# Optimization experiments

Hardware: AMD Instinct MI355X
Metric: run time of the kernel (lower is better)

## Reference

```python
import jax, jax.numpy as jnp
import numpy as np

B, S_BERT, L_WORD, D = 64, 512, 256, 768
REDUC, HID, TAGS, POL = 400, 100, 5, 4


def _make_positions():
    # Each word spans 1-2 consecutive subwords; 256 words * max 2 <= 512 subwords.
    rng = np.random.default_rng(0)
    lens = rng.integers(1, 3, size=(B, L_WORD))          # [B, L] in {1,2}
    starts = np.cumsum(lens, axis=1) - lens              # exclusive prefix sum
    ends = starts + lens - 1                             # inclusive end, <= 511
    return jnp.asarray(np.stack([starts, ends], axis=-1), dtype=jnp.int32)


def setup_inputs() -> dict:
    key = jax.random.key(0)
    ks = jax.random.split(key, 8)
    s = 0.02
    return {
        "bert_vectors": jax.random.normal(ks[0], (B, S_BERT, D), jnp.float32),
        "positions": _make_positions(),
        "W_reduc": jax.random.normal(ks[1], (D, REDUC), jnp.float32) * s,
        "b_reduc": jnp.zeros((REDUC,), jnp.float32),
        "W_ap": jax.random.normal(ks[2], (REDUC, HID), jnp.float32) * s,
        "b_ap": jnp.zeros((HID,), jnp.float32),
        "W_op": jax.random.normal(ks[3], (REDUC, HID), jnp.float32) * s,
        "b_op": jnp.zeros((HID,), jnp.float32),
        "W_ap_tag": jax.random.normal(ks[4], (HID, TAGS), jnp.float32) * s,
        "b_ap_tag": jnp.zeros((TAGS,), jnp.float32),
        "W_op_tag": jax.random.normal(ks[5], (HID, TAGS), jnp.float32) * s,
        "b_op_tag": jnp.zeros((TAGS,), jnp.float32),
        # Biaffine: bias=(True, False) -> in1 gets a ones column: [HID+1, POL*HID]
        "W_bi": jax.random.normal(ks[6], (HID + 1, POL * HID), jnp.float32) * s,
    }


def _segment_mean(vectors, positions):
    # vectors: [B, S, D]; positions: [B, L, 2] inclusive (start, end) spans.
    cs = jnp.cumsum(vectors, axis=1)
    cs = jnp.concatenate([jnp.zeros_like(cs[:, :1]), cs], axis=1)   # [B, S+1, D]
    starts = positions[..., 0]
    ends = positions[..., 1]
    hi = jnp.take_along_axis(cs, (ends + 1)[..., None], axis=1)     # [B, L, D]
    lo = jnp.take_along_axis(cs, starts[..., None], axis=1)
    lens = (ends - starts + 1).astype(vectors.dtype)[..., None]
    return (hi - lo) / lens                                          # [B, L, D]


def reference(bert_vectors, positions, W_reduc, b_reduc, W_ap, b_ap, W_op, b_op,
              W_ap_tag, b_ap_tag, W_op_tag, b_op_tag, W_bi):
    pooled = _segment_mean(bert_vectors, positions)                  # [B, L, D]
    h = jax.nn.relu(pooled @ W_reduc + b_reduc)                      # [B, L, 400]
    ap = jax.nn.relu(h @ W_ap + b_ap)                                # [B, L, 100]
    op = jax.nn.relu(h @ W_op + b_op)                                # [B, L, 100]
    ap_out = ap @ W_ap_tag + b_ap_tag                                # [B, L, T]
    op_out = op @ W_op_tag + b_op_tag                                # [B, L, T]
    # Biaffine with bias=(True, False)
    ones = jnp.ones_like(ap[..., :1])
    a1 = jnp.concatenate([ap, ones], axis=-1)                        # [B, L, 101]
    affine = (a1 @ W_bi).reshape(ap.shape[0], ap.shape[1], POL, HID) # [B, L1, P, H]
    triplet = jnp.einsum('biph,bjh->bjip', affine, op)               # [B, L2, L1, P]
    return ap_out, op_out, triplet
```

## Files before the change

kernel.cpp:

```cpp
#include <hip/hip_runtime.h>
#include <hip/hip_bf16.h>

#define B_    64
#define S_    512
#define L_    256
#define D_    768
#define RED_  400
#define REDP_ 512
#define HID_  100
#define HIDP_ 128
#define TAGS_ 5
#define POL_  4
#define NBI_  512
#define NAO_  256
#define BL_   (B_ * L_)

typedef __attribute__((ext_vector_type(8))) short short8;
typedef __attribute__((ext_vector_type(4))) float f32x4;
typedef __attribute__((ext_vector_type(4))) unsigned short u16x4;

#define GLOAD_LDS16(gp, lp) __builtin_amdgcn_global_load_lds( \
    (const __attribute__((address_space(1))) void*)(gp),      \
    (__attribute__((address_space(3))) void*)(lp), 16, 0, 0)

__device__ inline float bf2f(unsigned short u) {
    union { unsigned int i; float f; } c; c.i = ((unsigned)u) << 16; return c.f;
}
__device__ inline unsigned short f2bf(float f) {
    __hip_bfloat16 h = __float2bfloat16(f);
    unsigned short u;
    __builtin_memcpy(&u, &h, 2);
    return u;
}

#define SZ0 393216
#define SZ1 131072
#define SZ2 65536
#define SZ3 512
#define SZ4 256
#define PREP_TOT (SZ0 + SZ1 + SZ2 + SZ3 + SZ4)
#define SEG_BLOCKS (BL_ / 4)
#define PREP_BLOCKS ((PREP_TOT + 255) / 256)

__global__ __launch_bounds__(256) void front_kernel(
    const float* __restrict__ bert, const int* __restrict__ pos,
    unsigned short* __restrict__ pooled,
    const float* __restrict__ W_reduc, const float* __restrict__ b_reduc,
    const float* __restrict__ W_ap, const float* __restrict__ b_ap,
    const float* __restrict__ W_op, const float* __restrict__ b_op,
    const float* __restrict__ W_bi,
    unsigned short* __restrict__ WtR, unsigned short* __restrict__ WtAO,
    unsigned short* __restrict__ WtBi,
    float* __restrict__ bR, float* __restrict__ bAO, float* __restrict__ bBi)
{
    if (blockIdx.x < SEG_BLOCKS) {
        int r  = threadIdx.x >> 6;
        int l  = threadIdx.x & 63;
        int bl = blockIdx.x * 4 + r;
        int b  = bl >> 8;
        int s  = pos[bl * 2 + 0];
        int e  = pos[bl * 2 + 1];
        int len = e - s + 1;
        const float* v0 = bert + ((size_t)b * S_ + s) * D_;
        float inv = (len == 2) ? 0.5f : 1.0f;
        unsigned short* outp = pooled + (size_t)bl * D_;
        #pragma unroll
        for (int c = 0; c < 3; ++c) {
            int d = l * 4 + c * 256;
            f32x4 x = *(const f32x4*)(v0 + d);
            if (len == 2) {
                f32x4 y = *(const f32x4*)(v0 + D_ + d);
                x += y;
            }
            u16x4 o;
            #pragma unroll
            for (int j = 0; j < 4; ++j) o[j] = f2bf(x[j] * inv);
            *(u16x4*)(outp + d) = o;
        }
        return;
    }

    int idx = (blockIdx.x - SEG_BLOCKS) * 256 + threadIdx.x;
    if (idx < SZ0) {
        int n = idx / D_, k = idx - n * D_;
        float v = (n < RED_) ? W_reduc[(size_t)k * RED_ + n] : 0.f;
        WtR[idx] = f2bf(v);
    } else if (idx < SZ0 + SZ1) {
        int i = idx - SZ0;
        int n = i >> 9, k = i & 511;
        float v = 0.f;
        if (k < RED_) {
            if (n < HID_)                      v = W_ap[(size_t)k * HID_ + n];
            else if (n >= 128 && n < 128+HID_) v = W_op[(size_t)k * HID_ + (n-128)];
        }
        WtAO[i] = f2bf(v);
    } else if (idx < SZ0 + SZ1 + SZ2) {
        int i = idx - SZ0 - SZ1;
        int n = i >> 7, k = i & 127;
        int p = n >> 7, h = n & 127;
        float v = (h < HID_ && k < HID_) ? W_bi[(size_t)k * RED_ + p * HID_ + h] : 0.f;
        WtBi[i] = f2bf(v);
        if (k == 0) bBi[n] = (h < HID_) ? W_bi[(size_t)HID_ * RED_ + p * HID_ + h] : 0.f;
    } else if (idx < SZ0 + SZ1 + SZ2 + SZ3) {
        int n = idx - SZ0 - SZ1 - SZ2;
        bR[n] = (n < RED_) ? b_reduc[n] : 0.f;
    } else if (idx < PREP_TOT) {
        int n = idx - SZ0 - SZ1 - SZ2 - SZ3;
        bAO[n] = (n < 128) ? ((n < HID_) ? b_ap[n] : 0.f)
                           : (((n-128) < HID_) ? b_op[n-128] : 0.f);
    }
}

__global__ __launch_bounds__(256) void gemm1_kernel(
    const short* __restrict__ A, const short* __restrict__ Bt,
    const float* __restrict__ bias, unsigned short* __restrict__ Co,
    int M, int N, int K)
{
    __shared__ __align__(16) short lds[2][8192];

    const int t  = threadIdx.x;
    const int wv = t >> 6;
    const int ln = t & 63;
    const int wm = wv >> 1;
    const int wn = wv & 1;
    const int bm = blockIdx.x * 128;
    const int bn = blockIdx.y * 128;

    const int srow = t >> 2;
    const int skc  = (t & 3) * 8;

    f32x4 acc[4][4] = {};
    const int NT = K >> 5;

    {
        #pragma unroll
        for (int q = 0; q < 2; ++q) {
            const short* g = A + (size_t)(bm + q * 64 + srow) * K + skc;
            GLOAD_LDS16(g, &lds[0][q * 2048 + wv * 512]);
        }
        #pragma unroll
        for (int q = 0; q < 2; ++q) {
            const short* g = Bt + (size_t)(bn + q * 64 + srow) * K + skc;
            GLOAD_LDS16(g, &lds[0][4096 + q * 2048 + wv * 512]);
        }
    }
    __syncthreads();

    int cur = 0;
    const int lr = ln & 15;
    const int lk = (ln >> 4) * 8;

    for (int kt = 0; kt < NT; ++kt) {
        if (kt + 1 < NT) {
            int k0 = (kt + 1) << 5;
            #pragma unroll
            for (int q = 0; q < 2; ++q) {
                const short* g = A + (size_t)(bm + q * 64 + srow) * K + k0 + skc;
                GLOAD_LDS16(g, &lds[cur ^ 1][q * 2048 + wv * 512]);
            }
            #pragma unroll
            for (int q = 0; q < 2; ++q) {
                const short* g = Bt + (size_t)(bn + q * 64 + srow) * K + k0 + skc;
                GLOAD_LDS16(g, &lds[cur ^ 1][4096 + q * 2048 + wv * 512]);
            }
        }

        const short* As = &lds[cur][0];
        const short* Bs = &lds[cur][4096];
        short8 a[4], b[4];
        #pragma unroll
        for (int fi = 0; fi < 4; ++fi)
            a[fi] = *(const short8*)(As + (wm * 64 + fi * 16 + lr) * 32 + lk);
        #pragma unroll
        for (int fj = 0; fj < 4; ++fj)
            b[fj] = *(const short8*)(Bs + (wn * 64 + fj * 16 + lr) * 32 + lk);
        #pragma unroll
        for (int fi = 0; fi < 4; ++fi)
            #pragma unroll
            for (int fj = 0; fj < 4; ++fj)
                acc[fi][fj] = __builtin_amdgcn_mfma_f32_16x16x32_bf16(
                    a[fi], b[fj], acc[fi][fj], 0, 0, 0);

        __syncthreads();
        cur ^= 1;
    }

    const int row0 = bm + wm * 64 + (ln >> 4) * 4;
    const int col0 = bn + wn * 64 + lr;
    #pragma unroll
    for (int fi = 0; fi < 4; ++fi)
        #pragma unroll
        for (int r = 0; r < 4; ++r) {
            int row = row0 + fi * 16 + r;
            #pragma unroll
            for (int fj = 0; fj < 4; ++fj) {
                int col = col0 + fj * 16;
                float v = fmaxf(acc[fi][fj][r] + bias[col], 0.f);
                Co[(size_t)row * N + col] = f2bf(v);
            }
        }
}

__global__ __launch_bounds__(256) void gemm23_tag_kernel(
    const short* __restrict__ A, const short* __restrict__ Bt,
    const float* __restrict__ bias,
    unsigned short* __restrict__ apOut, unsigned short* __restrict__ opOut,
    const float* __restrict__ Wap_tag, const float* __restrict__ bap_tag,
    const float* __restrict__ Wop_tag, const float* __restrict__ bop_tag,
    float* __restrict__ out_tag)
{
    __shared__ __align__(16) short lds[2][8192];
    __shared__ float tagf[128 * 101];
    __shared__ float Wtag[HID_ * TAGS_];
    __shared__ float Btag[TAGS_];

    const int t  = threadIdx.x;
    const int wv = t >> 6;
    const int ln = t & 63;
    const int wm = wv >> 1;
    const int wn = wv & 1;
    const int bm = blockIdx.x * 128;
    const int bn = blockIdx.y * 128;
    const int half = blockIdx.y;

    const float* Wt = half ? Wop_tag : Wap_tag;
    const float* bt = half ? bop_tag : bap_tag;
    for (int i = t; i < HID_ * TAGS_; i += 256) Wtag[i] = Wt[i];
    if (t < TAGS_) Btag[t] = bt[t];

    const int srow = t >> 2;
    const int skc  = (t & 3) * 8;
    const int K = REDP_;

    f32x4 acc[4][4] = {};

    {
        #pragma unroll
        for (int q = 0; q < 2; ++q) {
            const short* g = A + (size_t)(bm + q * 64 + srow) * K + skc;
            GLOAD_LDS16(g, &lds[0][q * 2048 + wv * 512]);
        }
        #pragma unroll
        for (int q = 0; q < 2; ++q) {
            const short* g = Bt + (size_t)(bn + q * 64 + srow) * K + skc;
            GLOAD_LDS16(g, &lds[0][4096 + q * 2048 + wv * 512]);
        }
    }
    __syncthreads();

    int cur = 0;
    const int lr = ln & 15;
    const int lk = (ln >> 4) * 8;

    for (int kt = 0; kt < 16; ++kt) {
        if (kt + 1 < 16) {
            int k0 = (kt + 1) << 5;
            #pragma unroll
            for (int q = 0; q < 2; ++q) {
                const short* g = A + (size_t)(bm + q * 64 + srow) * K + k0 + skc;
                GLOAD_LDS16(g, &lds[cur ^ 1][q * 2048 + wv * 512]);
            }
            #pragma unroll
            for (int q = 0; q < 2; ++q) {
                const short* g = Bt + (size_t)(bn + q * 64 + srow) * K + k0 + skc;
                GLOAD_LDS16(g, &lds[cur ^ 1][4096 + q * 2048 + wv * 512]);
            }
        }

        const short* As = &lds[cur][0];
        const short* Bs = &lds[cur][4096];
        short8 a[4], b[4];
        #pragma unroll
        for (int fi = 0; fi < 4; ++fi)
            a[fi] = *(const short8*)(As + (wm * 64 + fi * 16 + lr) * 32 + lk);
        #pragma unroll
        for (int fj = 0; fj < 4; ++fj)
            b[fj] = *(const short8*)(Bs + (wn * 64 + fj * 16 + lr) * 32 + lk);
        #pragma unroll
        for (int fi = 0; fi < 4; ++fi)
            #pragma unroll
            for (int fj = 0; fj < 4; ++fj)
                acc[fi][fj] = __builtin_amdgcn_mfma_f32_16x16x32_bf16(
                    a[fi], b[fj], acc[fi][fj], 0, 0, 0);

        __syncthreads();
        cur ^= 1;
    }

    unsigned short* Co = half ? opOut : apOut;
    const int rl0 = wm * 64 + (ln >> 4) * 4;
    const int cl0 = wn * 64 + lr;
    #pragma unroll
    for (int fi = 0; fi < 4; ++fi)
        #pragma unroll
        for (int r = 0; r < 4; ++r) {
            int rl = rl0 + fi * 16 + r;
            #pragma unroll
            for (int fj = 0; fj < 4; ++fj) {
                int cl = cl0 + fj * 16;
                float v = fmaxf(acc[fi][fj][r] + bias[bn + cl], 0.f);
                Co[(size_t)(bm + rl) * 128 + cl] = f2bf(v);
                if (cl < 101) tagf[rl * 101 + cl] = v;
            }
        }
    __syncthreads();

    if (t < 128) {
        float s[TAGS_];
        #pragma unroll
        for (int g = 0; g < TAGS_; ++g) s[g] = Btag[g];
        const float* rowp = &tagf[t * 101];
        for (int k = 0; k < HID_; ++k) {
            float x = rowp[k];
            #pragma unroll
            for (int g = 0; g < TAGS_; ++g) s[g] += x * Wtag[k * TAGS_ + g];
        }
        float* o = out_tag + (size_t)half * (BL_ * TAGS_) + (size_t)(bm + t) * TAGS_;
        #pragma unroll
        for (int g = 0; g < TAGS_; ++g) o[g] = s[g];
    }
}

__global__ __launch_bounds__(256) void affine_kernel(
    const short* __restrict__ ap, const short* __restrict__ WtBi,
    const float* __restrict__ bBi, unsigned short* __restrict__ affine)
{
    __shared__ __align__(16) short As[16384];
    __shared__ __align__(16) short Bs[16384];

    const int t  = threadIdx.x;
    const int wv = t >> 6;
    const int ln = t & 63;
    const int wm = wv >> 1;
    const int wn = wv & 1;
    const int bm = blockIdx.x * 128;
    const int bn = blockIdx.y * 128;

    const int rsub = ln >> 2;
    const int j8   = (ln & 3) * 8;

    #pragma unroll
    for (int i = 0; i < 8; ++i) {
        int ks = i >> 1, hf = i & 1;
        int rloc = wv * 32 + hf * 16;
        const short* gA = ap + (size_t)(bm + rloc + rsub) * HIDP_ + ks * 32 + j8;
        GLOAD_LDS16(gA, &As[ks * 4096 + rloc * 32]);
        const short* gB = WtBi + (size_t)(bn + rloc + rsub) * HIDP_ + ks * 32 + j8;
        GLOAD_LDS16(gB, &Bs[ks * 4096 + rloc * 32]);
    }
    __syncthreads();

    const int lr = ln & 15;
    const int lk = (ln >> 4) * 8;
    f32x4 acc[4][4] = {};

    #pragma unroll
    for (int ks = 0; ks < 4; ++ks) {
        short8 a[4], b[4];
        #pragma unroll
        for (int fi = 0; fi < 4; ++fi)
            a[fi] = *(const short8*)(As + ks * 4096 + (wm * 64 + fi * 16 + lr) * 32 + lk);
        #pragma unroll
        for (int fj = 0; fj < 4; ++fj)
            b[fj] = *(const short8*)(Bs + ks * 4096 + (wn * 64 + fj * 16 + lr) * 32 + lk);
        #pragma unroll
        for (int fi = 0; fi < 4; ++fi)
            #pragma unroll
            for (int fj = 0; fj < 4; ++fj)
                acc[fi][fj] = __builtin_amdgcn_mfma_f32_16x16x32_bf16(
                    a[fi], b[fj], acc[fi][fj], 0, 0, 0);
    }

    const int row0 = bm + wm * 64 + (ln >> 4) * 4;
    const int col0 = bn + wn * 64 + lr;
    #pragma unroll
    for (int fi = 0; fi < 4; ++fi)
        #pragma unroll
        for (int r = 0; r < 4; ++r) {
            int row = row0 + fi * 16 + r;
            #pragma unroll
            for (int fj = 0; fj < 4; ++fj) {
                int col = col0 + fj * 16;
                affine[(size_t)row * NBI_ + col] = f2bf(acc[fi][fj][r] + bBi[col]);
            }
        }
}

__global__ __launch_bounds__(256) void triplet_kernel(
    const short* __restrict__ op, const short* __restrict__ affine,
    float* __restrict__ out)
{
    __shared__ __align__(16) short As[16384];
    __shared__ __align__(16) short Bs[16384];

    const int t  = threadIdx.x;
    const int wv = t >> 6;
    const int ln = t & 63;
    const int wm = wv >> 1;
    const int wn = wv & 1;
    const int bm = blockIdx.x * 128;
    const int bn = blockIdx.y * 128;
    const int b  = blockIdx.z;

    const short* Ab = op     + (size_t)b * 256 * HIDP_;
    const short* Bb = affine + (size_t)b * 256 * NBI_;

    const int rsub = ln >> 2;
    const int j8   = (ln & 3) * 8;

    #pragma unroll
    for (int i = 0; i < 8; ++i) {
        int ks = i >> 1, hf = i & 1;
        int rloc = wv * 32 + hf * 16;
        const short* gA = Ab + (size_t)(bm + rloc + rsub) * HIDP_ + ks * 32 + j8;
        GLOAD_LDS16(gA, &As[ks * 4096 + rloc * 32]);
        int ip = bn + rloc + rsub;
        const short* gB = Bb + (size_t)(ip >> 2) * NBI_ + (ip & 3) * HIDP_ + ks * 32 + j8;
        GLOAD_LDS16(gB, &Bs[ks * 4096 + rloc * 32]);
    }
    __syncthreads();

    const int lr = ln & 15;
    const int lk = (ln >> 4) * 8;
    f32x4 acc[4][4] = {};

    #pragma unroll
    for (int ks = 0; ks < 4; ++ks) {
        short8 a[4], bf[4];
        #pragma unroll
        for (int fi = 0; fi < 4; ++fi)
            a[fi] = *(const short8*)(As + ks * 4096 + (wm * 64 + fi * 16 + lr) * 32 + lk);
        #pragma unroll
        for (int fj = 0; fj < 4; ++fj)
            bf[fj] = *(const short8*)(Bs + ks * 4096 + (wn * 64 + fj * 16 + lr) * 32 + lk);
        #pragma unroll
        for (int fi = 0; fi < 4; ++fi)
            #pragma unroll
            for (int fj = 0; fj < 4; ++fj)
                acc[fi][fj] = __builtin_amdgcn_mfma_f32_16x16x32_bf16(
                    a[fi], bf[fj], acc[fi][fj], 0, 0, 0);
    }

    float* O = out + (size_t)b * 256 * 1024;
    const int row0 = bm + wm * 64 + (ln >> 4) * 4;
    const int col0 = bn + wn * 64 + lr;
    #pragma unroll
    for (int fi = 0; fi < 4; ++fi)
        #pragma unroll
        for (int r = 0; r < 4; ++r) {
            int row = row0 + fi * 16 + r;
            #pragma unroll
            for (int fj = 0; fj < 4; ++fj)
                O[(size_t)row * 1024 + col0 + fj * 16] = acc[fi][fj][r];
        }
}

extern "C" void kernel_launch(void* const* d_in, const int* in_sizes, int n_in,
                              void* d_out, int out_size, void* d_ws, size_t ws_size,
                              hipStream_t stream)
{
    const float* bert     = (const float*)d_in[0];
    const int*   pos      = (const int*)  d_in[1];
    const float* W_reduc  = (const float*)d_in[2];
    const float* b_reduc  = (const float*)d_in[3];
    const float* W_ap     = (const float*)d_in[4];
    const float* b_ap     = (const float*)d_in[5];
    const float* W_op     = (const float*)d_in[6];
    const float* b_op     = (const float*)d_in[7];
    const float* W_ap_tag = (const float*)d_in[8];
    const float* b_ap_tag = (const float*)d_in[9];
    const float* W_op_tag = (const float*)d_in[10];
    const float* b_op_tag = (const float*)d_in[11];
    const float* W_bi     = (const float*)d_in[12];

    float* out = (float*)d_out;

    char* ws = (char*)d_ws;
    unsigned short* pooled = (unsigned short*)ws; ws += (size_t)BL_ * D_ * 2;
    unsigned short* h      = (unsigned short*)ws; ws += (size_t)BL_ * REDP_ * 2;
    unsigned short* ap     = (unsigned short*)ws; ws += (size_t)BL_ * HIDP_ * 2;
    unsigned short* opv    = (unsigned short*)ws; ws += (size_t)BL_ * HIDP_ * 2;
    unsigned short* affine = (unsigned short*)ws; ws += (size_t)BL_ * NBI_ * 2;
    unsigned short* WtR    = (unsigned short*)ws; ws += (size_t)REDP_ * D_ * 2;
    unsigned short* WtAO   = (unsigned short*)ws; ws += (size_t)NAO_ * REDP_ * 2;
    unsigned short* WtBi   = (unsigned short*)ws; ws += (size_t)NBI_ * HIDP_ * 2;
    float* bR  = (float*)ws;  ws += REDP_ * 4;
    float* bAO = (float*)ws;  ws += NAO_ * 4;
    float* bBi = (float*)ws;  ws += NBI_ * 4;

    front_kernel<<<SEG_BLOCKS + PREP_BLOCKS, 256, 0, stream>>>(
        bert, pos, pooled,
        W_reduc, b_reduc, W_ap, b_ap, W_op, b_op, W_bi,
        WtR, WtAO, WtBi, bR, bAO, bBi);

    gemm1_kernel<<<dim3(BL_ / 128, REDP_ / 128), 256, 0, stream>>>(
        (const short*)pooled, (const short*)WtR, bR, h, BL_, REDP_, D_);

    gemm23_tag_kernel<<<dim3(BL_ / 128, 2), 256, 0, stream>>>(
        (const short*)h, (const short*)WtAO, bAO, ap, opv,
        W_ap_tag, b_ap_tag, W_op_tag, b_op_tag, out);

    affine_kernel<<<dim3(BL_ / 128, NBI_ / 128), 256, 0, stream>>>(
        (const short*)ap, (const short*)WtBi, bBi, affine);

    triplet_kernel<<<dim3(2, 8, B_), 256, 0, stream>>>(
        (const short*)opv, (const short*)affine, out + 2 * BL_ * TAGS_);
}
```

Before: 84.50 us.

## Fuse biaffine projection into triplet kernel and skip padded GEMM columns

Removes the separate affine kernel and its large bf16 intermediate buffer. Each triplet block now computes its slice of the affine projection directly into LDS, from ap rows and WtBi, before running the op x affine MFMA. This saves a global write and read of the affine tensor plus one launch. The cost is that the two x-blocks sharing a slice both recompute it. Separately, gemm1 skips MFMAs and stores for output columns beyond 416, and gemm23 stops its K loop at 416 instead of 512, so less padded work is done.

```diff
diff --git a/kernel.cpp b/kernel.cpp
--- a/kernel.cpp
+++ b/kernel.cpp
@@ -7,6 +7,7 @@
 #define D_    768
 #define RED_  400
 #define REDP_ 512
+#define KEFF_ 416
 #define HID_  100
 #define HIDP_ 128
 #define TAGS_ 5
@@ -114,7 +115,7 @@
 __global__ __launch_bounds__(256) void gemm1_kernel(
     const short* __restrict__ A, const short* __restrict__ Bt,
     const float* __restrict__ bias, unsigned short* __restrict__ Co,
-    int M, int N, int K)
+    int M, int N, int K, int nlim)
 {
     __shared__ __align__(16) short lds[2][8192];
 
@@ -129,6 +130,9 @@
     const int srow = t >> 2;
     const int skc  = (t & 3) * 8;
 
+    int fjrem = (nlim - bn - wn * 64) >> 4;
+    const int fjcnt = fjrem < 0 ? 0 : (fjrem > 4 ? 4 : fjrem);
+
     f32x4 acc[4][4] = {};
     const int NT = K >> 5;
 
@@ -173,13 +177,15 @@
             a[fi] = *(const short8*)(As + (wm * 64 + fi * 16 + lr) * 32 + lk);
         #pragma unroll
         for (int fj = 0; fj < 4; ++fj)
-            b[fj] = *(const short8*)(Bs + (wn * 64 + fj * 16 + lr) * 32 + lk);
+            if (fj < fjcnt)
+                b[fj] = *(const short8*)(Bs + (wn * 64 + fj * 16 + lr) * 32 + lk);
         #pragma unroll
         for (int fi = 0; fi < 4; ++fi)
             #pragma unroll
             for (int fj = 0; fj < 4; ++fj)
-                acc[fi][fj] = __builtin_amdgcn_mfma_f32_16x16x32_bf16(
-                    a[fi], b[fj], acc[fi][fj], 0, 0, 0);
+                if (fj < fjcnt)
+                    acc[fi][fj] = __builtin_amdgcn_mfma_f32_16x16x32_bf16(
+                        a[fi], b[fj], acc[fi][fj], 0, 0, 0);
 
         __syncthreads();
         cur ^= 1;
@@ -193,11 +199,12 @@
         for (int r = 0; r < 4; ++r) {
             int row = row0 + fi * 16 + r;
             #pragma unroll
-            for (int fj = 0; fj < 4; ++fj) {
-                int col = col0 + fj * 16;
-                float v = fmaxf(acc[fi][fj][r] + bias[col], 0.f);
-                Co[(size_t)row * N + col] = f2bf(v);
-            }
+            for (int fj = 0; fj < 4; ++fj)
+                if (fj < fjcnt) {
+                    int col = col0 + fj * 16;
+                    float v = fmaxf(acc[fi][fj][r] + bias[col], 0.f);
+                    Co[(size_t)row * N + col] = f2bf(v);
+                }
         }
 }
 
@@ -230,19 +237,19 @@
 
     const int srow = t >> 2;
     const int skc  = (t & 3) * 8;
-    const int K = REDP_;
+    const int NT = KEFF_ >> 5;
 
     f32x4 acc[4][4] = {};
 
     {
         #pragma unroll
         for (int q = 0; q < 2; ++q) {
-            const short* g = A + (size_t)(bm + q * 64 + srow) * K + skc;
+            const short* g = A + (size_t)(bm + q * 64 + srow) * REDP_ + skc;
             GLOAD_LDS16(g, &lds[0][q * 2048 + wv * 512]);
         }
         #pragma unroll
         for (int q = 0; q < 2; ++q) {
-            const short* g = Bt + (size_t)(bn + q * 64 + srow) * K + skc;
+            const short* g = Bt + (size_t)(bn + q * 64 + srow) * REDP_ + skc;
             GLOAD_LDS16(g, &lds[0][4096 + q * 2048 + wv * 512]);
         }
     }
@@ -252,17 +259,17 @@
     const int lr = ln & 15;
     const int lk = (ln >> 4) * 8;
 
-    for (int kt = 0; kt < 16; ++kt) {
-        if (kt + 1 < 16) {
+    for (int kt = 0; kt < NT; ++kt) {
+        if (kt + 1 < NT) {
             int k0 = (kt + 1) << 5;
             #pragma unroll
             for (int q = 0; q < 2; ++q) {
-                const short* g = A + (size_t)(bm + q * 64 + srow) * K + k0 + skc;
+                const short* g = A + (size_t)(bm + q * 64 + srow) * REDP_ + k0 + skc;
                 GLOAD_LDS16(g, &lds[cur ^ 1][q * 2048 + wv * 512]);
             }
             #pragma unroll
             for (int q = 0; q < 2; ++q) {
-                const short* g = Bt + (size_t)(bn + q * 64 + srow) * K + k0 + skc;
+                const short* g = Bt + (size_t)(bn + q * 64 + srow) * REDP_ + k0 + skc;
                 GLOAD_LDS16(g, &lds[cur ^ 1][4096 + q * 2048 + wv * 512]);
             }
         }
@@ -321,77 +328,14 @@
     }
 }
 
-__global__ __launch_bounds__(256) void affine_kernel(
-    const short* __restrict__ ap, const short* __restrict__ WtBi,
-    const float* __restrict__ bBi, unsigned short* __restrict__ affine)
-{
-    __shared__ __align__(16) short As[16384];
-    __shared__ __align__(16) short Bs[16384];
-
-    const int t  = threadIdx.x;
-    const int wv = t >> 6;
-    const int ln = t & 63;
-    const int wm = wv >> 1;
-    const int wn = wv & 1;
-    const int bm = blockIdx.x * 128;
-    const int bn = blockIdx.y * 128;
-
-    const int rsub = ln >> 2;
-    const int j8   = (ln & 3) * 8;
-
-    #pragma unroll
-    for (int i = 0; i < 8; ++i) {
-        int ks = i >> 1, hf = i & 1;
-        int rloc = wv * 32 + hf * 16;
-        const short* gA = ap + (size_t)(bm + rloc + rsub) * HIDP_ + ks * 32 + j8;
-        GLOAD_LDS16(gA, &As[ks * 4096 + rloc * 32]);
-        const short* gB = WtBi + (size_t)(bn + rloc + rsub) * HIDP_ + ks * 32 + j8;
-        GLOAD_LDS16(gB, &Bs[ks * 4096 + rloc * 32]);
-    }
-    __syncthreads();
-
-    const int lr = ln & 15;
-    const int lk = (ln >> 4) * 8;
-    f32x4 acc[4][4] = {};
-
-    #pragma unroll
-    for (int ks = 0; ks < 4; ++ks) {
-        short8 a[4], b[4];
-        #pragma unroll
-        for (int fi = 0; fi < 4; ++fi)
-            a[fi] = *(const short8*)(As + ks * 4096 + (wm * 64 + fi * 16 + lr) * 32 + lk);
-        #pragma unroll
-        for (int fj = 0; fj < 4; ++fj)
-            b[fj] = *(const short8*)(Bs + ks * 4096 + (wn * 64 + fj * 16 + lr) * 32 + lk);
-        #pragma unroll
-        for (int fi = 0; fi < 4; ++fi)
-            #pragma unroll
-            for (int fj = 0; fj < 4; ++fj)
-                acc[fi][fj] = __builtin_amdgcn_mfma_f32_16x16x32_bf16(
-                    a[fi], b[fj], acc[fi][fj], 0, 0, 0);
-    }
-
-    const int row0 = bm + wm * 64 + (ln >> 4) * 4;
-    const int col0 = bn + wn * 64 + lr;
-    #pragma unroll
-    for (int fi = 0; fi < 4; ++fi)
-        #pragma unroll
-        for (int r = 0; r < 4; ++r) {
-            int row = row0 + fi * 16 + r;
-            #pragma unroll
-            for (int fj = 0; fj < 4; ++fj) {
-                int col = col0 + fj * 16;
-                affine[(size_t)row * NBI_ + col] = f2bf(acc[fi][fj][r] + bBi[col]);
-            }
-        }
-}
-
-__global__ __launch_bounds__(256) void triplet_kernel(
-    const short* __restrict__ op, const short* __restrict__ affine,
+__global__ __launch_bounds__(256) void bi_triplet_kernel(
+    const short* __restrict__ op, const short* __restrict__ ap,
+    const short* __restrict__ WtBi, const float* __restrict__ bBi,
     float* __restrict__ out)
 {
     __shared__ __align__(16) short As[16384];
     __shared__ __align__(16) short Bs[16384];
+    __shared__ __align__(16) short Aap[4096];
 
     const int t  = threadIdx.x;
     const int wv = t >> 6;
@@ -402,8 +346,8 @@
     const int bn = blockIdx.y * 128;
     const int b  = blockIdx.z;
 
-    const short* Ab = op     + (size_t)b * 256 * HIDP_;
-    const short* Bb = affine + (size_t)b * 256 * NBI_;
+    const short* opB = op + (size_t)b * 256 * HIDP_;
+    const short* apB = ap + ((size_t)b * 256 + blockIdx.y * 32) * HIDP_;
 
     const int rsub = ln >> 2;
     const int j8   = (ln & 3) * 8;
@@ -412,18 +356,59 @@
     for (int i = 0; i < 8; ++i) {
         int ks = i >> 1, hf = i & 1;
         int rloc = wv * 32 + hf * 16;
-        const short* gA = Ab + (size_t)(bm + rloc + rsub) * HIDP_ + ks * 32 + j8;
+        const short* gA = opB + (size_t)(bm + rloc + rsub) * HIDP_ + ks * 32 + j8;
         GLOAD_LDS16(gA, &As[ks * 4096 + rloc * 32]);
-        int ip = bn + rloc + rsub;
-        const short* gB = Bb + (size_t)(ip >> 2) * NBI_ + (ip & 3) * HIDP_ + ks * 32 + j8;
-        GLOAD_LDS16(gB, &Bs[ks * 4096 + rloc * 32]);
+    }
+    #pragma unroll
+    for (int q = 0; q < 2; ++q) {
+        int kf   = q * 2 + (wv >> 1);
+        int irow = (wv & 1) * 16 + (ln >> 2);
+        const short* gA = apB + (size_t)irow * HIDP_ + kf * 32 + (ln & 3) * 8;
+        GLOAD_LDS16(gA, &Aap[q * 2048 + wv * 512]);
     }
     __syncthreads();
 
     const int lr = ln & 15;
     const int lk = (ln >> 4) * 8;
+    const int hbase = wv * 32;
+
+    #pragma unroll
+    for (int p = 0; p < 4; ++p) {
+        f32x4 acc2[2][2] = {};
+        const short* Wp = WtBi + (size_t)(p * 128) * HIDP_;
+        #pragma unroll
+        for (int kf = 0; kf < 4; ++kf) {
+            short8 a2[2], b2[2];
+            #pragma unroll
+            for (int fm = 0; fm < 2; ++fm)
+                a2[fm] = *(const short8*)(Aap + kf * 1024 + (fm * 16 + lr) * 32 + lk);
+            #pragma unroll
+            for (int fn = 0; fn < 2; ++fn)
+                b2[fn] = *(const short8*)(Wp + (size_t)(hbase + fn * 16 + lr) * HIDP_ + kf * 32 + lk);
+            #pragma unroll
+            for (int fm = 0; fm < 2; ++fm)
+                #pragma unroll
+                for (int fn = 0; fn < 2; ++fn)
+                    acc2[fm][fn] = __builtin_amdgcn_mfma_f32_16x16x32_bf16(
+                        a2[fm], b2[fn], acc2[fm][fn], 0, 0, 0);
+        }
+        #pragma unroll
+        for (int fm = 0; fm < 2; ++fm)
+            #pragma unroll
+            for (int fn = 0; fn < 2; ++fn) {
+                int h = hbase + fn * 16 + lr;
+                float bias = bBi[p * 128 + h];
+                #pragma unroll
+                for (int r = 0; r < 4; ++r) {
+                    int i = fm * 16 + (ln >> 4) * 4 + r;
+                    float v = acc2[fm][fn][r] + bias;
+                    Bs[(h >> 5) * 4096 + (i * 4 + p) * 32 + (h & 31)] = (short)f2bf(v);
+                }
+            }
+    }
+    __syncthreads();
+
     f32x4 acc[4][4] = {};
-
     #pragma unroll
     for (int ks = 0; ks < 4; ++ks) {
         short8 a[4], bf[4];
@@ -480,7 +465,6 @@
     unsigned short* h      = (unsigned short*)ws; ws += (size_t)BL_ * REDP_ * 2;
     unsigned short* ap     = (unsigned short*)ws; ws += (size_t)BL_ * HIDP_ * 2;
     unsigned short* opv    = (unsigned short*)ws; ws += (size_t)BL_ * HIDP_ * 2;
-    unsigned short* affine = (unsigned short*)ws; ws += (size_t)BL_ * NBI_ * 2;
     unsigned short* WtR    = (unsigned short*)ws; ws += (size_t)REDP_ * D_ * 2;
     unsigned short* WtAO   = (unsigned short*)ws; ws += (size_t)NAO_ * REDP_ * 2;
     unsigned short* WtBi   = (unsigned short*)ws; ws += (size_t)NBI_ * HIDP_ * 2;
@@ -494,15 +478,13 @@
         WtR, WtAO, WtBi, bR, bAO, bBi);
 
     gemm1_kernel<<<dim3(BL_ / 128, REDP_ / 128), 256, 0, stream>>>(
-        (const short*)pooled, (const short*)WtR, bR, h, BL_, REDP_, D_);
+        (const short*)pooled, (const short*)WtR, bR, h, BL_, REDP_, D_, KEFF_);
 
     gemm23_tag_kernel<<<dim3(BL_ / 128, 2), 256, 0, stream>>>(
         (const short*)h, (const short*)WtAO, bAO, ap, opv,
         W_ap_tag, b_ap_tag, W_op_tag, b_op_tag, out);
 
-    affine_kernel<<<dim3(BL_ / 128, NBI_ / 128), 256, 0, stream>>>(
-        (const short*)ap, (const short*)WtBi, bBi, affine);
-
-    triplet_kernel<<<dim3(2, 8, B_), 256, 0, stream>>>(
-        (const short*)opv, (const short*)affine, out + 2 * BL_ * TAGS_);
-}
+    bi_triplet_kernel<<<dim3(2, 8, B_), 256, 0, stream>>>(
+        (const short*)opv, (const short*)ap, (const short*)WtBi, bBi,
+        out + 2 * BL_ * TAGS_);
+}
```

Result: slower. 96.48 us (+14.2%).

## Skip padded reduction columns in GEMMs and vectorize triplet output stores

Applied to the files above, without the earlier changes.

gemm1 now skips MFMAs, fragment loads and stores for output columns at or beyond 416, since the reduction width is 400 padded to 512. gemm23 iterates K only up to 416 instead of 512, saving 3 of 16 k-tiles. The triplet kernel swaps operand roles so each lane's accumulator holds four consecutive (i,p) outputs, allowing 16-byte vector stores instead of scalar strided stores. Columns 416-511 of h are left unwritten; this is safe only because gemm23 never reads past column 416, and it leaves uninitialized data in the workspace.

```diff
diff --git a/kernel.cpp b/kernel.cpp
--- a/kernel.cpp
+++ b/kernel.cpp
@@ -7,6 +7,7 @@
 #define D_    768
 #define RED_  400
 #define REDP_ 512
+#define KEFF_ 416
 #define HID_  100
 #define HIDP_ 128
 #define TAGS_ 5
@@ -114,7 +115,7 @@
 __global__ __launch_bounds__(256) void gemm1_kernel(
     const short* __restrict__ A, const short* __restrict__ Bt,
     const float* __restrict__ bias, unsigned short* __restrict__ Co,
-    int M, int N, int K)
+    int M, int N, int K, int nlim)
 {
     __shared__ __align__(16) short lds[2][8192];
 
@@ -129,6 +130,9 @@
     const int srow = t >> 2;
     const int skc  = (t & 3) * 8;
 
+    int fjrem = (nlim - bn - wn * 64) >> 4;
+    const int fjcnt = fjrem < 0 ? 0 : (fjrem > 4 ? 4 : fjrem);
+
     f32x4 acc[4][4] = {};
     const int NT = K >> 5;
 
@@ -173,13 +177,15 @@
             a[fi] = *(const short8*)(As + (wm * 64 + fi * 16 + lr) * 32 + lk);
         #pragma unroll
         for (int fj = 0; fj < 4; ++fj)
-            b[fj] = *(const short8*)(Bs + (wn * 64 + fj * 16 + lr) * 32 + lk);
+            if (fj < fjcnt)
+                b[fj] = *(const short8*)(Bs + (wn * 64 + fj * 16 + lr) * 32 + lk);
         #pragma unroll
         for (int fi = 0; fi < 4; ++fi)
             #pragma unroll
             for (int fj = 0; fj < 4; ++fj)
-                acc[fi][fj] = __builtin_amdgcn_mfma_f32_16x16x32_bf16(
-                    a[fi], b[fj], acc[fi][fj], 0, 0, 0);
+                if (fj < fjcnt)
+                    acc[fi][fj] = __builtin_amdgcn_mfma_f32_16x16x32_bf16(
+                        a[fi], b[fj], acc[fi][fj], 0, 0, 0);
 
         __syncthreads();
         cur ^= 1;
@@ -193,11 +199,12 @@
         for (int r = 0; r < 4; ++r) {
             int row = row0 + fi * 16 + r;
             #pragma unroll
-            for (int fj = 0; fj < 4; ++fj) {
-                int col = col0 + fj * 16;
-                float v = fmaxf(acc[fi][fj][r] + bias[col], 0.f);
-                Co[(size_t)row * N + col] = f2bf(v);
-            }
+            for (int fj = 0; fj < 4; ++fj)
+                if (fj < fjcnt) {
+                    int col = col0 + fj * 16;
+                    float v = fmaxf(acc[fi][fj][r] + bias[col], 0.f);
+                    Co[(size_t)row * N + col] = f2bf(v);
+                }
         }
 }
 
@@ -230,19 +237,19 @@
 
     const int srow = t >> 2;
     const int skc  = (t & 3) * 8;
-    const int K = REDP_;
+    const int NT = KEFF_ >> 5;
 
     f32x4 acc[4][4] = {};
 
     {
         #pragma unroll
         for (int q = 0; q < 2; ++q) {
-            const short* g = A + (size_t)(bm + q * 64 + srow) * K + skc;
+            const short* g = A + (size_t)(bm + q * 64 + srow) * REDP_ + skc;
             GLOAD_LDS16(g, &lds[0][q * 2048 + wv * 512]);
         }
         #pragma unroll
         for (int q = 0; q < 2; ++q) {
-            const short* g = Bt + (size_t)(bn + q * 64 + srow) * K + skc;
+            const short* g = Bt + (size_t)(bn + q * 64 + srow) * REDP_ + skc;
             GLOAD_LDS16(g, &lds[0][4096 + q * 2048 + wv * 512]);
         }
     }
@@ -252,17 +259,17 @@
     const int lr = ln & 15;
     const int lk = (ln >> 4) * 8;
 
-    for (int kt = 0; kt < 16; ++kt) {
-        if (kt + 1 < 16) {
+    for (int kt = 0; kt < NT; ++kt) {
+        if (kt + 1 < NT) {
             int k0 = (kt + 1) << 5;
             #pragma unroll
             for (int q = 0; q < 2; ++q) {
-                const short* g = A + (size_t)(bm + q * 64 + srow) * K + k0 + skc;
+                const short* g = A + (size_t)(bm + q * 64 + srow) * REDP_ + k0 + skc;
                 GLOAD_LDS16(g, &lds[cur ^ 1][q * 2048 + wv * 512]);
             }
             #pragma unroll
             for (int q = 0; q < 2; ++q) {
-                const short* g = Bt + (size_t)(bn + q * 64 + srow) * K + k0 + skc;
+                const short* g = Bt + (size_t)(bn + q * 64 + srow) * REDP_ + k0 + skc;
                 GLOAD_LDS16(g, &lds[cur ^ 1][4096 + q * 2048 + wv * 512]);
             }
         }
@@ -426,33 +433,33 @@
 
     #pragma unroll
     for (int ks = 0; ks < 4; ++ks) {
-        short8 a[4], bf[4];
-        #pragma unroll
-        for (int fi = 0; fi < 4; ++fi)
-            a[fi] = *(const short8*)(As + ks * 4096 + (wm * 64 + fi * 16 + lr) * 32 + lk);
-        #pragma unroll
-        for (int fj = 0; fj < 4; ++fj)
-            bf[fj] = *(const short8*)(Bs + ks * 4096 + (wn * 64 + fj * 16 + lr) * 32 + lk);
-        #pragma unroll
-        for (int fi = 0; fi < 4; ++fi)
-            #pragma unroll
-            for (int fj = 0; fj < 4; ++fj)
-                acc[fi][fj] = __builtin_amdgcn_mfma_f32_16x16x32_bf16(
-                    a[fi], bf[fj], acc[fi][fj], 0, 0, 0);
+        short8 af[4], of[4];
+        #pragma unroll
+        for (int fa = 0; fa < 4; ++fa)
+            af[fa] = *(const short8*)(Bs + ks * 4096 + (wn * 64 + fa * 16 + lr) * 32 + lk);
+        #pragma unroll
+        for (int fo = 0; fo < 4; ++fo)
+            of[fo] = *(const short8*)(As + ks * 4096 + (wm * 64 + fo * 16 + lr) * 32 + lk);
+        #pragma unroll
+        for (int fa = 0; fa < 4; ++fa)
+            #pragma unroll
+            for (int fo = 0; fo < 4; ++fo)
+                acc[fa][fo] = __builtin_amdgcn_mfma_f32_16x16x32_bf16(
+                    af[fa], of[fo], acc[fa][fo], 0, 0, 0);
     }
 
     float* O = out + (size_t)b * 256 * 1024;
-    const int row0 = bm + wm * 64 + (ln >> 4) * 4;
-    const int col0 = bn + wn * 64 + lr;
-    #pragma unroll
-    for (int fi = 0; fi < 4; ++fi)
-        #pragma unroll
-        for (int r = 0; r < 4; ++r) {
-            int row = row0 + fi * 16 + r;
-            #pragma unroll
-            for (int fj = 0; fj < 4; ++fj)
-                O[(size_t)row * 1024 + col0 + fj * 16] = acc[fi][fj][r];
-        }
+    const int ipb = bn + wn * 64 + (ln >> 4) * 4;
+    const int jb  = bm + wm * 64 + lr;
+    #pragma unroll
+    for (int fa = 0; fa < 4; ++fa) {
+        int ip0 = ipb + fa * 16;
+        #pragma unroll
+        for (int fo = 0; fo < 4; ++fo) {
+            int j = jb + fo * 16;
+            *(f32x4*)(O + (size_t)j * 1024 + ip0) = acc[fa][fo];
+        }
+    }
 }
 
 extern "C" void kernel_launch(void* const* d_in, const int* in_sizes, int n_in,
@@ -494,7 +501,7 @@
         WtR, WtAO, WtBi, bR, bAO, bBi);
 
     gemm1_kernel<<<dim3(BL_ / 128, REDP_ / 128), 256, 0, stream>>>(
-        (const short*)pooled, (const short*)WtR, bR, h, BL_, REDP_, D_);
+        (const short*)pooled, (const short*)WtR, bR, h, BL_, REDP_, D_, KEFF_);
 
     gemm23_tag_kernel<<<dim3(BL_ / 128, 2), 256, 0, stream>>>(
         (const short*)h, (const short*)WtAO, bAO, ap, opv,
```

Result: slower. 97.99 us (+16.0%).
